# Kernel optimization log

Measured on AMD Instinct MI355X. Metric: run time of the kernel, lower is better.

Reference implementation:

```python
import jax, jax.numpy as jnp
import numpy as np


def setup_inputs() -> dict:
    key = jax.random.key(0)
    k1, k2, k3, k4 = jax.random.split(key, 4)
    B, n_env, in_ch, out_ch, code_ch, modes1, L = 16, 8, 32, 32, 16, 64, 8192
    scale = 1.0 / (in_ch * out_ch)
    return {
        "x": jax.random.normal(k1, (B, n_env * in_ch, L), dtype=jnp.float32),
        "codes": jax.random.normal(k2, (n_env, code_ch), dtype=jnp.float32),
        "com_weights": scale * jax.random.uniform(k3, (in_ch, out_ch, modes1, 2), dtype=jnp.float32),
        "code_weights": scale * jax.random.uniform(k4, (code_ch * in_ch, out_ch, modes1, 2), dtype=jnp.float32),
        "filter_weights": -3.0 * jnp.ones((modes1,), dtype=jnp.float32),
    }


def _as_complex(w):
    return w[..., 0] + 1j * w[..., 1]


def reference(x, codes, com_weights, code_weights, filter_weights):
    B, C, L = x.shape
    n_env, code_ch = codes.shape
    in_ch = C // n_env
    out_ch = com_weights.shape[1]
    modes1 = com_weights.shape[2]
    n_freq = L // 2 + 1

    # FFT and reshape to [B, e, i, freq]
    x_ft = jnp.fft.rfft(x).reshape(B, n_env, in_ch, n_freq)
    xm = x_ft[..., :modes1]  # mode truncation

    cw = _as_complex(com_weights)  # [i, o, m]
    codew = _as_complex(code_weights.reshape(code_ch, in_ch, out_ch, modes1, 2))  # [c,i,o,m]
    env_w = jnp.einsum('ec,ciom->eiom', codes.astype(codew.dtype), codew)

    # hardsigmoid(filter_weights): clip(x/6 + 0.5, 0, 1)
    lam = jnp.clip(filter_weights / 6.0 + 0.5, 0.0, 1.0)  # [m]

    out_m = (lam * jnp.einsum('beim,iom->beom', xm, cw)
             + (1.0 - lam) * jnp.einsum('beim,eiom->beom', xm, env_w))  # [B,e,o,m]

    # zero-pad back to full spectrum then inverse FFT
    out_ft = jnp.zeros((B, n_env, out_ch, n_freq), dtype=out_m.dtype)
    out_ft = out_ft.at[..., :modes1].set(out_m)
    out_ft = out_ft.reshape(B, n_env * out_ch, n_freq)
    return jnp.fft.irfft(out_ft, n=L)
```

## Files before the change

### kernel.cpp

```cpp
#include <hip/hip_runtime.h>
#include <hip/hip_bf16.h>
#include <math.h>
#include <stdint.h>

typedef __bf16 bf16_t;
typedef __bf16 bf16x8 __attribute__((ext_vector_type(8)));
typedef float  f32x4  __attribute__((ext_vector_type(4)));

#define L_LEN 8192
#define MODES 64
#define NCOMP 128
#define M_ROWS 4096

__device__ __forceinline__ void g2lds16(const void* g, void* l) {
  __builtin_amdgcn_global_load_lds(
      (__attribute__((address_space(1))) void*)(uintptr_t)(g),
      (__attribute__((address_space(3))) void*)(l), 16, 0, 0);
}

__global__ void gen_basis(bf16_t* __restrict__ B1t, bf16_t* __restrict__ B1) {
  int id = blockIdx.x * 256 + threadIdx.x;
  int l = id >> 6;
  int k = id & 63;
  int r = (l * k) & (L_LEN - 1);
  float ang = (float)r * 7.6699039394282061e-4f;
  float s, c;
  sincosf(ang, &s, &c);
  B1 [l * NCOMP + k]             = (bf16_t)c;
  B1 [l * NCOMP + MODES + k]     = (bf16_t)(-s);
  B1t[(size_t)k * L_LEN + l]           = (bf16_t)c;
  B1t[(size_t)(MODES + k) * L_LEN + l] = (bf16_t)(-s);
}

__global__ void wmix(const float* __restrict__ codes, const float* __restrict__ comw,
                     const float* __restrict__ codew, const float* __restrict__ fw,
                     float* __restrict__ W) {
  int id = blockIdx.x * 256 + threadIdx.x;
  int k = id & 63;
  int o = (id >> 6) & 31;
  int i = (id >> 11) & 31;
  int e = id >> 16;
  float lam = fminf(fmaxf(fw[k] * (1.0f / 6.0f) + 0.5f, 0.0f), 1.0f);
  float are = 0.f, aim = 0.f;
#pragma unroll
  for (int c = 0; c < 16; ++c) {
    float cd = codes[e * 16 + c];
    const float* p = codew + ((((c * 32 + i) * 32 + o) * 64 + k) << 1);
    are += cd * p[0];
    aim += cd * p[1];
  }
  const float* q = comw + (((i * 32 + o) * 64 + k) << 1);
  float wre = lam * q[0] + (1.f - lam) * are;
  float wim = lam * q[1] + (1.f - lam) * aim;
  float* dst = W + ((((e * 32 + i) * 32 + o) * 64 + k) << 1);
  dst[0] = wre;
  dst[1] = wim;
}

__global__ __launch_bounds__(256) void stage1(const float* __restrict__ x,
                                              const bf16_t* __restrict__ B1t,
                                              float* __restrict__ X) {
  __shared__ bf16_t Al[128 * 72];
  __shared__ bf16_t Bl[128 * 64];
  const int t = threadIdx.x;
  const int lane = t & 63;
  const int w = t >> 6;
  const int wm = w >> 1, wn = w & 1;
  const int mt = blockIdx.x;
  const int sp = blockIdx.y;
  const int lq = lane >> 4;
  const int l15 = lane & 15;

  f32x4 acc[4][4];
#pragma unroll
  for (int a = 0; a < 4; ++a)
#pragma unroll
    for (int b = 0; b < 4; ++b) acc[a][b] = (f32x4){0.f, 0.f, 0.f, 0.f};

  const int r = t >> 1, half = t & 1;
  const float* xrow = x + (size_t)(mt * 128 + r) * L_LEN + half * 32;
  bf16_t* adst = Al + r * 72 + half * 32;

  for (int ch = 0; ch < 8; ++ch) {
    const int l0 = sp * 512 + ch * 64;
    __syncthreads();
    const float4* xp = (const float4*)(xrow + l0);
#pragma unroll
    for (int j = 0; j < 4; ++j) {
      float4 p0 = xp[2 * j], p1 = xp[2 * j + 1];
      bf16x8 v = {(bf16_t)p0.x, (bf16_t)p0.y, (bf16_t)p0.z, (bf16_t)p0.w,
                  (bf16_t)p1.x, (bf16_t)p1.y, (bf16_t)p1.z, (bf16_t)p1.w};
      *(bf16x8*)(adst + j * 8) = v;
    }
#pragma unroll
    for (int q2 = 0; q2 < 4; ++q2) {
      int slot = t + 256 * q2;
      int n  = slot >> 3;
      int m8 = slot & 7;
      int j8 = m8 ^ (n & 7);
      g2lds16(B1t + (size_t)n * L_LEN + l0 + j8 * 8, (char*)Bl + slot * 16);
    }
    __syncthreads();
#pragma unroll
    for (int s = 0; s < 2; ++s) {
      bf16x8 a[4], b[4];
#pragma unroll
      for (int mf = 0; mf < 4; ++mf) {
        int row = wm * 64 + mf * 16 + l15;
        a[mf] = *(const bf16x8*)(Al + row * 72 + s * 32 + lq * 8);
      }
#pragma unroll
      for (int nf = 0; nf < 4; ++nf) {
        int n = wn * 64 + nf * 16 + l15;
        int j8 = (s * 4 + lq) ^ (n & 7);
        b[nf] = *(const bf16x8*)(Bl + n * 64 + j8 * 8);
      }
#pragma unroll
      for (int mf = 0; mf < 4; ++mf)
#pragma unroll
        for (int nf = 0; nf < 4; ++nf)
          acc[mf][nf] = __builtin_amdgcn_mfma_f32_16x16x32_bf16(a[mf], b[nf], acc[mf][nf], 0, 0, 0);
    }
  }
#pragma unroll
  for (int mf = 0; mf < 4; ++mf)
#pragma unroll
    for (int nf = 0; nf < 4; ++nf) {
      int n = wn * 64 + nf * 16 + l15;
#pragma unroll
      for (int rg = 0; rg < 4; ++rg) {
        int m = mt * 128 + wm * 64 + mf * 16 + lq * 4 + rg;
        atomicAdd(X + (size_t)m * NCOMP + n, acc[mf][nf][rg]);
      }
    }
}

__global__ __launch_bounds__(256) void mixk(const float* __restrict__ X,
                                            const float* __restrict__ W,
                                            bf16_t* __restrict__ A2) {
  __shared__ float Xs[32 * 128];
  const int t = threadIdx.x;
  const int be = blockIdx.x;
  const int e = be & 7;
#pragma unroll
  for (int j = 0; j < 16; ++j) {
    int idx = t + 256 * j;
    Xs[idx] = X[(size_t)be * 4096 + idx];
  }
  __syncthreads();
  const int k = t & 63;
  const int olo = t >> 6;
  float yre[8], yim[8];
#pragma unroll
  for (int j = 0; j < 8; ++j) { yre[j] = 0.f; yim[j] = 0.f; }
  for (int i = 0; i < 32; ++i) {
    float xr = Xs[i * 128 + k];
    float xi = Xs[i * 128 + 64 + k];
    const float* wp = W + ((((e * 32 + i) * 32 + olo * 8) * 64 + k) << 1);
#pragma unroll
    for (int j = 0; j < 8; ++j) {
      float2 wv = *(const float2*)(wp + j * 128);
      yre[j] += xr * wv.x - xi * wv.y;
      yim[j] += xr * wv.y + xi * wv.x;
    }
  }
  float sc = (k == 0) ? (1.0f / 8192.0f) : (2.0f / 8192.0f);
#pragma unroll
  for (int j = 0; j < 8; ++j) {
    int m = be * 32 + olo * 8 + j;
    A2[m * NCOMP + k]         = (bf16_t)(yre[j] * sc);
    A2[m * NCOMP + MODES + k] = (bf16_t)(yim[j] * sc);
  }
}

__global__ __launch_bounds__(256) void stage2(const bf16_t* __restrict__ A2,
                                              const bf16_t* __restrict__ B1,
                                              float* __restrict__ out) {
  __shared__ bf16_t As[128 * 128];
  __shared__ bf16_t Bs[128 * 128];
  const int t = threadIdx.x;
  const int lane = t & 63;
  const int w = t >> 6;
  const int wm = w >> 1, wl = w & 1;
  const int lt = blockIdx.x, mt = blockIdx.y;
  const int lq = lane >> 4, l15 = lane & 15;

#pragma unroll
  for (int q2 = 0; q2 < 8; ++q2) {
    int slot = t + 256 * q2;
    int row = slot >> 4;
    int m16 = slot & 15;
    int j8 = m16 ^ (row & 15);
    g2lds16(A2 + (size_t)(mt * 128 + row) * NCOMP + j8 * 8, (char*)As + slot * 16);
  }
#pragma unroll
  for (int q2 = 0; q2 < 8; ++q2) {
    int slot = t + 256 * q2;
    int lr = slot >> 4;
    int m16 = slot & 15;
    int j8 = m16 ^ (lr & 15);
    g2lds16(B1 + (size_t)(lt * 128 + lr) * NCOMP + j8 * 8, (char*)Bs + slot * 16);
  }
  __syncthreads();

  f32x4 acc[4][4];
#pragma unroll
  for (int a = 0; a < 4; ++a)
#pragma unroll
    for (int b = 0; b < 4; ++b) acc[a][b] = (f32x4){0.f, 0.f, 0.f, 0.f};

#pragma unroll
  for (int s = 0; s < 4; ++s) {
    bf16x8 a[4], b[4];
#pragma unroll
    for (int mf = 0; mf < 4; ++mf) {
      int row = wm * 64 + mf * 16 + l15;
      a[mf] = *(const bf16x8*)(As + row * 128 + (((s * 4 + lq) ^ (row & 15)) * 8));
    }
#pragma unroll
    for (int nf = 0; nf < 4; ++nf) {
      int lr = wl * 64 + nf * 16 + l15;
      b[nf] = *(const bf16x8*)(Bs + lr * 128 + (((s * 4 + lq) ^ (lr & 15)) * 8));
    }
#pragma unroll
    for (int mf = 0; mf < 4; ++mf)
#pragma unroll
      for (int nf = 0; nf < 4; ++nf)
        acc[mf][nf] = __builtin_amdgcn_mfma_f32_16x16x32_bf16(a[mf], b[nf], acc[mf][nf], 0, 0, 0);
  }

#pragma unroll
  for (int mf = 0; mf < 4; ++mf)
#pragma unroll
    for (int nf = 0; nf < 4; ++nf) {
      int m = mt * 128 + wm * 64 + mf * 16 + lq * 4;
      int l = lt * 128 + wl * 64 + nf * 16 + l15;
      float* op = out + (size_t)m * L_LEN + l;
#pragma unroll
      for (int rg = 0; rg < 4; ++rg) op[(size_t)rg * L_LEN] = acc[mf][nf][rg];
    }
}

extern "C" void kernel_launch(void* const* d_in, const int* in_sizes, int n_in,
                              void* d_out, int out_size, void* d_ws, size_t ws_size,
                              hipStream_t stream) {
  const float* x     = (const float*)d_in[0];
  const float* codes = (const float*)d_in[1];
  const float* comw  = (const float*)d_in[2];
  const float* codew = (const float*)d_in[3];
  const float* fw    = (const float*)d_in[4];
  float* out = (float*)d_out;
  char* ws = (char*)d_ws;
  bf16_t* B1t = (bf16_t*)(ws);
  bf16_t* B1  = (bf16_t*)(ws + (size_t)(2u << 20));
  float*  X   = (float*) (ws + (size_t)(4u << 20));
  float*  W   = (float*) (ws + (size_t)(6u << 20));
  bf16_t* A2  = (bf16_t*)(ws + (size_t)(10u << 20));

  gen_basis<<<2048, 256, 0, stream>>>(B1t, B1);
  wmix<<<2048, 256, 0, stream>>>(codes, comw, codew, fw, W);
  hipMemsetAsync(X, 0, (size_t)M_ROWS * NCOMP * sizeof(float), stream);
  stage1<<<dim3(32, 16), 256, 0, stream>>>(x, B1t, X);
  mixk<<<128, 256, 0, stream>>>(X, W, A2);
  stage2<<<dim3(64, 32), 256, 0, stream>>>(A2, B1, out);
}
```

Measured before the change: 305.6 us.

## Drop LDS staging in GEMMs, replace atomics with split-K partials, vectorize basis gen

Stage1 and stage2 now read operands straight from global memory into MFMA registers instead of staging tiles through LDS. Stage1 writes per-split partial sums to a buffer that mixk reduces, which replaces the atomicAdd reduction and the memset. gen_basis computes eight values per thread and writes them as vector stores. This removes LDS traffic, barriers and atomics, but relies on cache hits for operand reuse and adds partial-buffer traffic.

Result: slower. 368.9 us (+20.7%).

```diff
diff --git a/kernel.cpp b/kernel.cpp
--- a/kernel.cpp
+++ b/kernel.cpp
@@ -11,25 +11,42 @@
 #define MODES 64
 #define NCOMP 128
 #define M_ROWS 4096
-
-__device__ __forceinline__ void g2lds16(const void* g, void* l) {
-  __builtin_amdgcn_global_load_lds(
-      (__attribute__((address_space(1))) void*)(uintptr_t)(g),
-      (__attribute__((address_space(3))) void*)(l), 16, 0, 0);
-}
-
-__global__ void gen_basis(bf16_t* __restrict__ B1t, bf16_t* __restrict__ B1) {
-  int id = blockIdx.x * 256 + threadIdx.x;
-  int l = id >> 6;
-  int k = id & 63;
-  int r = (l * k) & (L_LEN - 1);
-  float ang = (float)r * 7.6699039394282061e-4f;
-  float s, c;
-  sincosf(ang, &s, &c);
-  B1 [l * NCOMP + k]             = (bf16_t)c;
-  B1 [l * NCOMP + MODES + k]     = (bf16_t)(-s);
-  B1t[(size_t)k * L_LEN + l]           = (bf16_t)c;
-  B1t[(size_t)(MODES + k) * L_LEN + l] = (bf16_t)(-s);
+#define SPLITS 16
+
+__global__ __launch_bounds__(256) void gen_basis(bf16_t* __restrict__ B1t,
+                                                 bf16_t* __restrict__ B1) {
+  const int id = blockIdx.x * 256 + threadIdx.x;
+  const float C0 = 7.6699039394282061e-4f;
+  if (id < 65536) {
+    const int l8 = id & 1023, k = id >> 10;
+    const int l0 = l8 * 8;
+    bf16x8 vc, vs;
+#pragma unroll
+    for (int j = 0; j < 8; ++j) {
+      int r = ((l0 + j) * k) & (L_LEN - 1);
+      float s, c;
+      sincosf((float)r * C0, &s, &c);
+      vc[j] = (bf16_t)c;
+      vs[j] = (bf16_t)(-s);
+    }
+    *(bf16x8*)(B1t + (size_t)k * L_LEN + l0)           = vc;
+    *(bf16x8*)(B1t + (size_t)(MODES + k) * L_LEN + l0) = vs;
+  } else {
+    const int id2 = id - 65536;
+    const int k8 = id2 & 7, l = id2 >> 3;
+    const int kk = k8 * 8;
+    bf16x8 vc, vs;
+#pragma unroll
+    for (int j = 0; j < 8; ++j) {
+      int r = (l * (kk + j)) & (L_LEN - 1);
+      float s, c;
+      sincosf((float)r * C0, &s, &c);
+      vc[j] = (bf16_t)c;
+      vs[j] = (bf16_t)(-s);
+    }
+    *(bf16x8*)(B1 + (size_t)l * NCOMP + kk)         = vc;
+    *(bf16x8*)(B1 + (size_t)l * NCOMP + MODES + kk) = vs;
+  }
 }
 
 __global__ void wmix(const float* __restrict__ codes, const float* __restrict__ comw,
@@ -59,93 +76,63 @@
 
 __global__ __launch_bounds__(256) void stage1(const float* __restrict__ x,
                                               const bf16_t* __restrict__ B1t,
-                                              float* __restrict__ X) {
-  __shared__ bf16_t Al[128 * 72];
-  __shared__ bf16_t Bl[128 * 64];
+                                              float* __restrict__ Xp) {
   const int t = threadIdx.x;
   const int lane = t & 63;
   const int w = t >> 6;
-  const int wm = w >> 1, wn = w & 1;
-  const int mt = blockIdx.x;
-  const int sp = blockIdx.y;
-  const int lq = lane >> 4;
-  const int l15 = lane & 15;
-
-  f32x4 acc[4][4];
-#pragma unroll
-  for (int a = 0; a < 4; ++a)
-#pragma unroll
-    for (int b = 0; b < 4; ++b) acc[a][b] = (f32x4){0.f, 0.f, 0.f, 0.f};
-
-  const int r = t >> 1, half = t & 1;
-  const float* xrow = x + (size_t)(mt * 128 + r) * L_LEN + half * 32;
-  bf16_t* adst = Al + r * 72 + half * 32;
-
-  for (int ch = 0; ch < 8; ++ch) {
-    const int l0 = sp * 512 + ch * 64;
-    __syncthreads();
-    const float4* xp = (const float4*)(xrow + l0);
-#pragma unroll
-    for (int j = 0; j < 4; ++j) {
-      float4 p0 = xp[2 * j], p1 = xp[2 * j + 1];
-      bf16x8 v = {(bf16_t)p0.x, (bf16_t)p0.y, (bf16_t)p0.z, (bf16_t)p0.w,
-                  (bf16_t)p1.x, (bf16_t)p1.y, (bf16_t)p1.z, (bf16_t)p1.w};
-      *(bf16x8*)(adst + j * 8) = v;
-    }
-#pragma unroll
-    for (int q2 = 0; q2 < 4; ++q2) {
-      int slot = t + 256 * q2;
-      int n  = slot >> 3;
-      int m8 = slot & 7;
-      int j8 = m8 ^ (n & 7);
-      g2lds16(B1t + (size_t)n * L_LEN + l0 + j8 * 8, (char*)Bl + slot * 16);
-    }
-    __syncthreads();
-#pragma unroll
-    for (int s = 0; s < 2; ++s) {
-      bf16x8 a[4], b[4];
-#pragma unroll
-      for (int mf = 0; mf < 4; ++mf) {
-        int row = wm * 64 + mf * 16 + l15;
-        a[mf] = *(const bf16x8*)(Al + row * 72 + s * 32 + lq * 8);
+  const int l15 = lane & 15, lq = lane >> 4;
+  const int m0 = blockIdx.x * 64 + w * 16;
+  const int k0 = blockIdx.y * 512;
+
+  const float*  ap = x   + (size_t)(m0 + l15) * L_LEN + k0 + lq * 8;
+  const bf16_t* bp = B1t + (size_t)l15 * L_LEN + k0 + lq * 8;
+
+  f32x4 acc[8];
+#pragma unroll
+  for (int nf = 0; nf < 8; ++nf) acc[nf] = (f32x4){0.f, 0.f, 0.f, 0.f};
+
+  for (int kk = 0; kk < 4; ++kk) {
+#pragma unroll
+    for (int s = 0; s < 4; ++s) {
+      const float4 p0 = *(const float4*)(ap + s * 32);
+      const float4 p1 = *(const float4*)(ap + s * 32 + 4);
+      bf16x8 av = {(bf16_t)p0.x, (bf16_t)p0.y, (bf16_t)p0.z, (bf16_t)p0.w,
+                   (bf16_t)p1.x, (bf16_t)p1.y, (bf16_t)p1.z, (bf16_t)p1.w};
+#pragma unroll
+      for (int nf = 0; nf < 8; ++nf) {
+        bf16x8 bv = *(const bf16x8*)(bp + (size_t)nf * (16 * L_LEN) + s * 32);
+        acc[nf] = __builtin_amdgcn_mfma_f32_16x16x32_bf16(av, bv, acc[nf], 0, 0, 0);
       }
-#pragma unroll
-      for (int nf = 0; nf < 4; ++nf) {
-        int n = wn * 64 + nf * 16 + l15;
-        int j8 = (s * 4 + lq) ^ (n & 7);
-        b[nf] = *(const bf16x8*)(Bl + n * 64 + j8 * 8);
-      }
-#pragma unroll
-      for (int mf = 0; mf < 4; ++mf)
-#pragma unroll
-        for (int nf = 0; nf < 4; ++nf)
-          acc[mf][nf] = __builtin_amdgcn_mfma_f32_16x16x32_bf16(a[mf], b[nf], acc[mf][nf], 0, 0, 0);
-    }
-  }
-#pragma unroll
-  for (int mf = 0; mf < 4; ++mf)
-#pragma unroll
-    for (int nf = 0; nf < 4; ++nf) {
-      int n = wn * 64 + nf * 16 + l15;
-#pragma unroll
-      for (int rg = 0; rg < 4; ++rg) {
-        int m = mt * 128 + wm * 64 + mf * 16 + lq * 4 + rg;
-        atomicAdd(X + (size_t)m * NCOMP + n, acc[mf][nf][rg]);
-      }
-    }
-}
-
-__global__ __launch_bounds__(256) void mixk(const float* __restrict__ X,
+    }
+    ap += 128;
+    bp += 128;
+  }
+
+  float* xout = Xp + (size_t)blockIdx.y * (M_ROWS * NCOMP) +
+                (size_t)(m0 + lq * 4) * NCOMP + l15;
+#pragma unroll
+  for (int nf = 0; nf < 8; ++nf)
+#pragma unroll
+    for (int rg = 0; rg < 4; ++rg)
+      xout[(size_t)rg * NCOMP + nf * 16] = acc[nf][rg];
+}
+
+__global__ __launch_bounds__(256) void mixk(const float* __restrict__ Xp,
                                             const float* __restrict__ W,
                                             bf16_t* __restrict__ A2) {
-  __shared__ float Xs[32 * 128];
+  __shared__ __align__(16) float Xs[32 * 128];
   const int t = threadIdx.x;
   const int be = blockIdx.x;
   const int e = be & 7;
-#pragma unroll
-  for (int j = 0; j < 16; ++j) {
-    int idx = t + 256 * j;
-    Xs[idx] = X[(size_t)be * 4096 + idx];
+  const float* xb = Xp + (size_t)be * (32 * NCOMP);
+#pragma unroll
+  for (int j = 0; j < 4; ++j) {
+    int idx = (t + 256 * j) * 4;
+    f32x4 s = (f32x4){0.f, 0.f, 0.f, 0.f};
+#pragma unroll
+    for (int sp = 0; sp < 16; ++sp)
+      s += *(const f32x4*)(xb + (size_t)sp * (M_ROWS * NCOMP) + idx);
+    *(f32x4*)(Xs + idx) = s;
   }
   __syncthreads();
   const int k = t & 63;
@@ -176,69 +163,36 @@
 __global__ __launch_bounds__(256) void stage2(const bf16_t* __restrict__ A2,
                                               const bf16_t* __restrict__ B1,
                                               float* __restrict__ out) {
-  __shared__ bf16_t As[128 * 128];
-  __shared__ bf16_t Bs[128 * 128];
   const int t = threadIdx.x;
   const int lane = t & 63;
   const int w = t >> 6;
-  const int wm = w >> 1, wl = w & 1;
-  const int lt = blockIdx.x, mt = blockIdx.y;
-  const int lq = lane >> 4, l15 = lane & 15;
-
-#pragma unroll
-  for (int q2 = 0; q2 < 8; ++q2) {
-    int slot = t + 256 * q2;
-    int row = slot >> 4;
-    int m16 = slot & 15;
-    int j8 = m16 ^ (row & 15);
-    g2lds16(A2 + (size_t)(mt * 128 + row) * NCOMP + j8 * 8, (char*)As + slot * 16);
-  }
-#pragma unroll
-  for (int q2 = 0; q2 < 8; ++q2) {
-    int slot = t + 256 * q2;
-    int lr = slot >> 4;
-    int m16 = slot & 15;
-    int j8 = m16 ^ (lr & 15);
-    g2lds16(B1 + (size_t)(lt * 128 + lr) * NCOMP + j8 * 8, (char*)Bs + slot * 16);
-  }
-  __syncthreads();
-
-  f32x4 acc[4][4];
-#pragma unroll
-  for (int a = 0; a < 4; ++a)
-#pragma unroll
-    for (int b = 0; b < 4; ++b) acc[a][b] = (f32x4){0.f, 0.f, 0.f, 0.f};
-
-#pragma unroll
+  const int l15 = lane & 15, lq = lane >> 4;
+  const int m0 = blockIdx.x * 64 + w * 16;
+  const int l0 = blockIdx.y * 128;
+
+  const bf16_t* apA = A2 + (size_t)(m0 + l15) * NCOMP + lq * 8;
+  const bf16_t* bpB = B1 + (size_t)(l0 + l15) * NCOMP + lq * 8;
+
+  f32x4 acc[8];
+#pragma unroll
+  for (int nf = 0; nf < 8; ++nf) acc[nf] = (f32x4){0.f, 0.f, 0.f, 0.f};
+
+#pragma unroll 2
   for (int s = 0; s < 4; ++s) {
-    bf16x8 a[4], b[4];
-#pragma unroll
-    for (int mf = 0; mf < 4; ++mf) {
-      int row = wm * 64 + mf * 16 + l15;
-      a[mf] = *(const bf16x8*)(As + row * 128 + (((s * 4 + lq) ^ (row & 15)) * 8));
-    }
-#pragma unroll
-    for (int nf = 0; nf < 4; ++nf) {
-      int lr = wl * 64 + nf * 16 + l15;
-      b[nf] = *(const bf16x8*)(Bs + lr * 128 + (((s * 4 + lq) ^ (lr & 15)) * 8));
-    }
-#pragma unroll
-    for (int mf = 0; mf < 4; ++mf)
-#pragma unroll
-      for (int nf = 0; nf < 4; ++nf)
-        acc[mf][nf] = __builtin_amdgcn_mfma_f32_16x16x32_bf16(a[mf], b[nf], acc[mf][nf], 0, 0, 0);
-  }
-
-#pragma unroll
-  for (int mf = 0; mf < 4; ++mf)
-#pragma unroll
-    for (int nf = 0; nf < 4; ++nf) {
-      int m = mt * 128 + wm * 64 + mf * 16 + lq * 4;
-      int l = lt * 128 + wl * 64 + nf * 16 + l15;
-      float* op = out + (size_t)m * L_LEN + l;
-#pragma unroll
-      for (int rg = 0; rg < 4; ++rg) op[(size_t)rg * L_LEN] = acc[mf][nf][rg];
-    }
+    bf16x8 av = *(const bf16x8*)(apA + s * 32);
+#pragma unroll
+    for (int nf = 0; nf < 8; ++nf) {
+      bf16x8 bv = *(const bf16x8*)(bpB + (size_t)nf * (16 * NCOMP) + s * 32);
+      acc[nf] = __builtin_amdgcn_mfma_f32_16x16x32_bf16(av, bv, acc[nf], 0, 0, 0);
+    }
+  }
+
+  float* op = out + (size_t)(m0 + lq * 4) * L_LEN + l0 + l15;
+#pragma unroll
+  for (int nf = 0; nf < 8; ++nf)
+#pragma unroll
+    for (int rg = 0; rg < 4; ++rg)
+      op[(size_t)rg * L_LEN + nf * 16] = acc[nf][rg];
 }
 
 extern "C" void kernel_launch(void* const* d_in, const int* in_sizes, int n_in,
@@ -253,14 +207,13 @@
   char* ws = (char*)d_ws;
   bf16_t* B1t = (bf16_t*)(ws);
   bf16_t* B1  = (bf16_t*)(ws + (size_t)(2u << 20));
-  float*  X   = (float*) (ws + (size_t)(4u << 20));
-  float*  W   = (float*) (ws + (size_t)(6u << 20));
-  bf16_t* A2  = (bf16_t*)(ws + (size_t)(10u << 20));
-
-  gen_basis<<<2048, 256, 0, stream>>>(B1t, B1);
+  float*  W   = (float*) (ws + (size_t)(4u << 20));
+  bf16_t* A2  = (bf16_t*)(ws + (size_t)(20u << 20));
+  float*  Xp  = (float*) (ws + (size_t)(24u << 20));
+
+  gen_basis<<<512, 256, 0, stream>>>(B1t, B1);
   wmix<<<2048, 256, 0, stream>>>(codes, comw, codew, fw, W);
-  hipMemsetAsync(X, 0, (size_t)M_ROWS * NCOMP * sizeof(float), stream);
-  stage1<<<dim3(32, 16), 256, 0, stream>>>(x, B1t, X);
-  mixk<<<128, 256, 0, stream>>>(X, W, A2);
-  stage2<<<dim3(64, 32), 256, 0, stream>>>(A2, B1, out);
-}
+  stage1<<<dim3(64, SPLITS), 256, 0, stream>>>(x, B1t, Xp);
+  mixk<<<128, 256, 0, stream>>>(Xp, W, A2);
+  stage2<<<dim3(64, 64), 256, 0, stream>>>(A2, B1, out);
+}
```
